# Optimization experiments

Hardware: AMD Instinct MI355X
Metric: run time of the kernel (lower is better)

The kernel has to match this reference:

```python
import jax, jax.numpy as jnp
import numpy as np

N_NODES = 100000
N_EDGES = 1600000
NFEAT, NHID, NCLASS = 512, 128, 16


def gcn_conv(x, edge_index, edge_weight, W, b):
    # Dense linear transform: [N, in] @ [in, out] -> [N, out]
    h = x @ W
    src, dst = edge_index[0], edge_index[1]
    # Edge-weighted gather + scatter-add (message passing)
    msgs = edge_weight[:, None] * h[src]            # [E, out]
    agg = jax.ops.segment_sum(msgs, dst, num_segments=x.shape[0])
    return agg + b


def setup_inputs() -> dict:
    key = jax.random.key(0)
    k = jax.random.split(key, 8)
    x = jax.random.normal(k[0], (N_NODES, NFEAT), dtype=jnp.float32)
    edge_index = jax.random.randint(k[1], (2, N_EDGES), 0, N_NODES, dtype=jnp.int64 if jax.config.jax_enable_x64 else jnp.int32)
    edge_weight = jax.random.uniform(k[2], (N_EDGES,), dtype=jnp.float32)
    # GCNConv glorot-initialized weights + zero biases
    s1 = np.sqrt(6.0 / (NFEAT + NHID)).astype(np.float32)
    s2 = np.sqrt(6.0 / (NHID + NCLASS)).astype(np.float32)
    W1 = jax.random.uniform(k[3], (NFEAT, NHID), minval=-s1, maxval=s1, dtype=jnp.float32)
    b1 = jnp.zeros((NHID,), dtype=jnp.float32)
    W2 = jax.random.uniform(k[4], (NHID, NCLASS), minval=-s2, maxval=s2, dtype=jnp.float32)
    b2 = jnp.zeros((NCLASS,), dtype=jnp.float32)
    return {"x": x, "edge_index": edge_index, "edge_weight": edge_weight,
            "W1": W1, "b1": b1, "W2": W2, "b2": b2}


def reference(x, edge_index, edge_weight, W1, b1, W2, b2):
    # GNNGuard.forward in eval mode (dropout is identity when not training)
    h = jax.nn.relu(gcn_conv(x, edge_index, edge_weight, W1, b1))
    out = gcn_conv(h, edge_index, edge_weight, W2, b2)
    return jax.nn.log_softmax(out, axis=1)
```

## Files before the change

### kernel.cpp

```cpp
#include <hip/hip_runtime.h>
#include <cstdint>
#include <cstddef>


#define NFEAT 512
#define NHID 128
#define NCLASS 16
#define MAXDEG 64
#define Q15 32768.0f
#define IQ15 3.0517578125e-05f

typedef __attribute__((ext_vector_type(8))) __bf16 bf16x8;
typedef __attribute__((ext_vector_type(4))) float f32x4;

__global__ void k_prep_w1(const float* __restrict__ W1, __bf16* __restrict__ W1f) {
    int t = blockIdx.x * 256 + threadIdx.x;
    if (t >= 16 * 8 * 64) return;
    int lane = t & 63;
    int nc = (t >> 6) & 7;
    int ks = t >> 9;
    int q = lane >> 4, col = lane & 15;
    __bf16* outp = W1f + (size_t)t * 8;
#pragma unroll
    for (int j = 0; j < 8; j++) {
        int k = ks * 32 + q * 8 + j;
        int n = nc * 16 + col;
        outp[j] = (__bf16)W1[k * NHID + n];
    }
}

__global__ void k_gemm1_scatter(const float* __restrict__ x, const __bf16* __restrict__ W1f,
                                __bf16* __restrict__ h1b, int M, int nG1, int nSc,
                                const int* __restrict__ src, const int* __restrict__ dst,
                                const float* __restrict__ ew, int* __restrict__ cnt,
                                uint32_t* __restrict__ pay, int E) {
    if ((int)blockIdx.x >= nG1) {
        int id = blockIdx.x - nG1;
        int stride = nSc << 8;
        int e0 = id * 256 + (int)threadIdx.x;
        int e1 = e0 + stride;
        bool v0 = e0 < E, v1 = e1 < E;
        int d0 = 0, s0 = 0, d1 = 0, s1 = 0;
        float w0 = 0.f, w1 = 0.f;
        if (v0) { d0 = dst[e0]; s0 = src[e0]; w0 = ew[e0]; }
        if (v1) { d1 = dst[e1]; s1 = src[e1]; w1 = ew[e1]; }
        int r0 = 0, r1 = 0;
        if (v0) r0 = atomicAdd(&cnt[d0], 1);
        if (v1) r1 = atomicAdd(&cnt[d1], 1);
        if (v0 && r0 < MAXDEG) {
            uint32_t q = (uint32_t)(w0 * Q15 + 0.5f);
            if (q > 32767u) q = 32767u;
            pay[(size_t)d0 * MAXDEG + r0] = ((uint32_t)s0 << 15) | q;
        }
        if (v1 && r1 < MAXDEG) {
            uint32_t q = (uint32_t)(w1 * Q15 + 0.5f);
            if (q > 32767u) q = 32767u;
            pay[(size_t)d1 * MAXDEG + r1] = ((uint32_t)s1 << 15) | q;
        }
        return;
    }
    int wave = threadIdx.x >> 6;
    int lane = threadIdx.x & 63;
    int q = lane >> 4;
    int col = lane & 15;
    int m0 = blockIdx.x * 64 + wave * 16 + col;
    bool valid = (m0 < M);

    f32x4 acc[8];
#pragma unroll
    for (int n = 0; n < 8; n++) acc[n] = (f32x4)(0.0f);

    const bf16x8* Bf = (const bf16x8*)W1f;
    const float* arow = x + (size_t)m0 * NFEAT + q * 8;

    for (int kk = 0; kk < NFEAT; kk += 32) {
        bf16x8 af;
        if (valid) {
            const f32x4* ap = (const f32x4*)(arow + kk);
            f32x4 a0 = __builtin_nontemporal_load(ap);
            f32x4 a1 = __builtin_nontemporal_load(ap + 1);
            af[0] = (__bf16)a0[0]; af[1] = (__bf16)a0[1];
            af[2] = (__bf16)a0[2]; af[3] = (__bf16)a0[3];
            af[4] = (__bf16)a1[0]; af[5] = (__bf16)a1[1];
            af[6] = (__bf16)a1[2]; af[7] = (__bf16)a1[3];
        } else {
#pragma unroll
            for (int j = 0; j < 8; j++) af[j] = (__bf16)0.0f;
        }
        int kb = (kk >> 5) * 8;
#pragma unroll
        for (int n = 0; n < 8; n++) {
            bf16x8 bf = Bf[(size_t)(kb + n) * 64 + lane];
            acc[n] = __builtin_amdgcn_mfma_f32_16x16x32_bf16(af, bf, acc[n], 0, 0, 0);
        }
    }

    int rbase = blockIdx.x * 64 + wave * 16 + q * 4;
#pragma unroll
    for (int r = 0; r < 4; r++) {
        int row = rbase + r;
        if (row < M) {
            __bf16* op = h1b + (size_t)row * NHID + col;
#pragma unroll
            for (int n = 0; n < 8; n++) op[n * 16] = (__bf16)acc[n][r];
        }
    }
}

__global__ void k_agg1(const uint32_t* __restrict__ h1u, const int* __restrict__ cnt,
                       const uint32_t* __restrict__ pay, const float* __restrict__ b1,
                       uint32_t* __restrict__ hu, int N) {
    int gw = (blockIdx.x * 256 + (int)threadIdx.x) >> 6;
    int lane = threadIdx.x & 63;
    if (gw >= N) return;
    const uint32_t* prow = pay + (size_t)gw * MAXDEG;
    uint32_t pv = prow[lane];
    int c = cnt[gw];
    if (c > MAXDEG) c = MAXDEG;
    int sv = (int)(pv >> 15);
    float wv = (lane < c) ? (float)(pv & 32767u) * IQ15 : 0.f;
    float ax = 0.f, ay = 0.f;
    int j = 0;
    for (; j + 8 <= c; j += 8) {
        uint32_t u[8];
        float w[8];
#pragma unroll
        for (int i = 0; i < 8; i++) {
            int s = __shfl(sv, j + i);
            w[i] = __shfl(wv, j + i);
            u[i] = h1u[(size_t)s * 64 + lane];
        }
#pragma unroll
        for (int i = 0; i < 8; i++) {
            ax = fmaf(w[i], __uint_as_float(u[i] << 16), ax);
            ay = fmaf(w[i], __uint_as_float(u[i] & 0xffff0000u), ay);
        }
    }
    for (; j + 4 <= c; j += 4) {
        uint32_t u[4];
        float w[4];
#pragma unroll
        for (int i = 0; i < 4; i++) {
            int s = __shfl(sv, j + i);
            w[i] = __shfl(wv, j + i);
            u[i] = h1u[(size_t)s * 64 + lane];
        }
#pragma unroll
        for (int i = 0; i < 4; i++) {
            ax = fmaf(w[i], __uint_as_float(u[i] << 16), ax);
            ay = fmaf(w[i], __uint_as_float(u[i] & 0xffff0000u), ay);
        }
    }
    for (; j < c; j++) {
        int s = __shfl(sv, j);
        float ww = __shfl(wv, j);
        uint32_t u = h1u[(size_t)s * 64 + lane];
        ax = fmaf(ww, __uint_as_float(u << 16), ax);
        ay = fmaf(ww, __uint_as_float(u & 0xffff0000u), ay);
    }
    float2 bb = ((const float2*)b1)[lane];
    float ox = fmaxf(ax + bb.x, 0.f);
    float oy = fmaxf(ay + bb.y, 0.f);
    union { __bf16 h[2]; uint32_t u; } cvt;
    cvt.h[0] = (__bf16)ox;
    cvt.h[1] = (__bf16)oy;
    hu[(size_t)gw * 64 + lane] = cvt.u;
}

__global__ void k_gemm2(const uint32_t* __restrict__ hu, const float* __restrict__ W2,
                        float* __restrict__ h2, int N) {
    __shared__ float W2s[NHID * NCLASS];
    __shared__ float hs[16][NHID + 4];
    int t = threadIdx.x;
#pragma unroll
    for (int j = 0; j < 8; j++) W2s[t * 8 + j] = W2[t * 8 + j];
    int nb = blockIdx.x * 16;
    {
        int idx = t * 4;
        int row = idx >> 6;
        int kp = idx & 63;
        if (nb + row < N) {
            uint4 u4 = *(const uint4*)(hu + (size_t)(nb + row) * 64 + kp);
            uint32_t us[4] = {u4.x, u4.y, u4.z, u4.w};
#pragma unroll
            for (int j = 0; j < 4; j++) {
                hs[row][(kp + j) * 2 + 0] = __uint_as_float(us[j] << 16);
                hs[row][(kp + j) * 2 + 1] = __uint_as_float(us[j] & 0xffff0000u);
            }
        } else {
#pragma unroll
            for (int j = 0; j < 4; j++) {
                hs[row][(kp + j) * 2 + 0] = 0.f;
                hs[row][(kp + j) * 2 + 1] = 0.f;
            }
        }
    }
    __syncthreads();
    int ni = t >> 4, c = t & 15;
    float acc = 0.f;
#pragma unroll 8
    for (int k = 0; k < NHID; k++) acc = fmaf(hs[ni][k], W2s[k * NCLASS + c], acc);
    if (nb + ni < N) h2[(size_t)(nb + ni) * NCLASS + c] = acc;
}

__global__ void k_agg2(const float* __restrict__ h2, const int* __restrict__ cnt,
                       const uint32_t* __restrict__ pay, const float* __restrict__ b2,
                       float* __restrict__ out, int N) {
    int gw = (blockIdx.x * 256 + (int)threadIdx.x) >> 6;
    int lane = threadIdx.x & 63;
    if (gw >= N) return;
    int c = lane & 15, eg = lane >> 4;
    const uint32_t* prow = pay + (size_t)gw * MAXDEG;
    uint32_t pv = prow[lane];
    int n = cnt[gw];
    if (n > MAXDEG) n = MAXDEG;
    int sv = (int)(pv >> 15);
    float wv = (lane < n) ? (float)(pv & 32767u) * IQ15 : 0.f;
    float acc = 0.f;
    int nr = (n + 3) >> 2;
    int i = 0;
    for (; i + 2 <= nr; i += 2) {
        int j0 = i * 4 + eg, j1 = j0 + 4;
        int s0 = __shfl(sv, j0), s1 = __shfl(sv, j1);
        float w0 = __shfl(wv, j0), w1 = __shfl(wv, j1);
        float g0 = h2[(size_t)s0 * NCLASS + c];
        float g1 = h2[(size_t)s1 * NCLASS + c];
        acc = fmaf(w0, g0, acc);
        acc = fmaf(w1, g1, acc);
    }
    if (i < nr) {
        int j0 = i * 4 + eg;
        int s0 = __shfl(sv, j0);
        float w0 = __shfl(wv, j0);
        acc = fmaf(w0, h2[(size_t)s0 * NCLASS + c], acc);
    }
    acc += __shfl_xor(acc, 16);
    acc += __shfl_xor(acc, 32);
    float o = acc + b2[c];
    float m = o;
#pragma unroll
    for (int d = 1; d < 16; d <<= 1) m = fmaxf(m, __shfl_xor(m, d));
    float e = expf(o - m);
    float ssum = e;
#pragma unroll
    for (int d = 1; d < 16; d <<= 1) ssum += __shfl_xor(ssum, d);
    if (lane < 16) out[(size_t)gw * NCLASS + c] = o - m - logf(ssum);
}

extern "C" void kernel_launch(void* const* d_in, const int* in_sizes, int n_in,
                              void* d_out, int out_size, void* d_ws, size_t ws_size,
                              hipStream_t stream) {
    const float* x  = (const float*)d_in[0];
    const int*   ei = (const int*)d_in[1];
    const float* ew = (const float*)d_in[2];
    const float* W1 = (const float*)d_in[3];
    const float* b1 = (const float*)d_in[4];
    const float* W2 = (const float*)d_in[5];
    const float* b2 = (const float*)d_in[6];
    float* out = (float*)d_out;

    int N = in_sizes[0] / NFEAT;
    int E = in_sizes[2];
    const int* srcI = ei;
    const int* dstI = ei + E;

    char* p = (char*)d_ws;
    auto alloc = [&](size_t bytes) {
        char* r = p;
        p += (bytes + 511) & ~(size_t)511;
        return r;
    };
    __bf16*   h1b  = (__bf16*)alloc((size_t)N * NHID * 2);
    uint32_t* hu   = (uint32_t*)alloc((size_t)N * (NHID / 2) * 4);
    float*    h2   = (float*)alloc((size_t)N * NCLASS * 4);
    int*      cnt  = (int*)alloc((size_t)N * 4);
    uint32_t* pay  = (uint32_t*)alloc((size_t)N * MAXDEG * 4);
    __bf16*   W1f  = (__bf16*)alloc((size_t)NFEAT * NHID * 2);

    (void)hipMemsetAsync(cnt, 0, (size_t)N * 4, stream);
    k_prep_w1<<<32, 256, 0, stream>>>(W1, W1f);

    int nG1 = (N + 63) / 64;
    int nSc = (E + 511) / 512;
    k_gemm1_scatter<<<nG1 + nSc, 256, 0, stream>>>(x, W1f, h1b, N, nG1, nSc,
                                                   srcI, dstI, ew, cnt, pay, E);

    k_agg1<<<(N + 3) / 4, 256, 0, stream>>>((const uint32_t*)h1b, cnt, pay, b1, hu, N);
    k_gemm2<<<(N + 15) / 16, 256, 0, stream>>>(hu, W2, h2, N);
    k_agg2<<<(N + 3) / 4, 256, 0, stream>>>(h2, cnt, pay, b2, out, N);
}
```

Baseline: 490.1 us.

## Process two nodes per wave in agg1 with 8-byte gathers; nontemporal payload stores

The first aggregation kernel now assigns two destination nodes to each 64-lane wave, each half-wave gathering a full 256-byte bf16 row with 8-byte loads per lane. This halves the number of waves and the per-edge shuffle and loop overhead relative to the feature work. The cost is that both halves iterate to the larger of the two degrees, with masked weights for the shorter node. Edge payload writes in the scatter phase also become nontemporal stores to reduce cache pollution.

```diff
diff --git a/kernel.cpp b/kernel.cpp
--- a/kernel.cpp
+++ b/kernel.cpp
@@ -50,12 +50,14 @@
         if (v0 && r0 < MAXDEG) {
             uint32_t q = (uint32_t)(w0 * Q15 + 0.5f);
             if (q > 32767u) q = 32767u;
-            pay[(size_t)d0 * MAXDEG + r0] = ((uint32_t)s0 << 15) | q;
+            __builtin_nontemporal_store(((uint32_t)s0 << 15) | q,
+                                        &pay[(size_t)d0 * MAXDEG + r0]);
         }
         if (v1 && r1 < MAXDEG) {
             uint32_t q = (uint32_t)(w1 * Q15 + 0.5f);
             if (q > 32767u) q = 32767u;
-            pay[(size_t)d1 * MAXDEG + r1] = ((uint32_t)s1 << 15) | q;
+            __builtin_nontemporal_store(((uint32_t)s1 << 15) | q,
+                                        &pay[(size_t)d1 * MAXDEG + r1]);
         }
         return;
     }
@@ -110,61 +112,84 @@
 __global__ void k_agg1(const uint32_t* __restrict__ h1u, const int* __restrict__ cnt,
                        const uint32_t* __restrict__ pay, const float* __restrict__ b1,
                        uint32_t* __restrict__ hu, int N) {
-    int gw = (blockIdx.x * 256 + (int)threadIdx.x) >> 6;
+    int wid = (blockIdx.x * 256 + (int)threadIdx.x) >> 6;
     int lane = threadIdx.x & 63;
-    if (gw >= N) return;
-    const uint32_t* prow = pay + (size_t)gw * MAXDEG;
-    uint32_t pv = prow[lane];
-    int c = cnt[gw];
-    if (c > MAXDEG) c = MAXDEG;
-    int sv = (int)(pv >> 15);
-    float wv = (lane < c) ? (float)(pv & 32767u) * IQ15 : 0.f;
-    float ax = 0.f, ay = 0.f;
+    int half = lane >> 5, hl = lane & 31;
+    int nA = wid * 2;
+    if (nA >= N) return;
+    int node = nA + half;
+    bool nodeValid = node < N;
+
+    uint32_t pv = nodeValid ? pay[(size_t)node * MAXDEG + hl] : 0u;
+    int c_own = 0;
+    if (nodeValid) { c_own = cnt[node]; if (c_own > MAXDEG) c_own = MAXDEG; }
+    int cA = __shfl(c_own, 0);
+    int cB = __shfl(c_own, 32);
+    int cmax = cA > cB ? cA : cB;
+    int cm32 = cmax < 32 ? cmax : 32;
+
+    const uint2* h1v = (const uint2*)h1u;
+    float a0 = 0.f, a1 = 0.f, a2 = 0.f, a3 = 0.f;
     int j = 0;
-    for (; j + 8 <= c; j += 8) {
-        uint32_t u[8];
+    for (; j + 8 <= cm32; j += 8) {
+        uint2 u[8];
         float w[8];
 #pragma unroll
         for (int i = 0; i < 8; i++) {
-            int s = __shfl(sv, j + i);
-            w[i] = __shfl(wv, j + i);
-            u[i] = h1u[(size_t)s * 64 + lane];
+            uint32_t pA = __shfl(pv, j + i);
+            uint32_t pB = __shfl(pv, 32 + j + i);
+            uint32_t p = half ? pB : pA;
+            int s = (int)(p >> 15);
+            w[i] = (j + i < c_own) ? (float)(p & 32767u) * IQ15 : 0.f;
+            u[i] = h1v[(size_t)s * 32 + hl];
         }
 #pragma unroll
         for (int i = 0; i < 8; i++) {
-            ax = fmaf(w[i], __uint_as_float(u[i] << 16), ax);
-            ay = fmaf(w[i], __uint_as_float(u[i] & 0xffff0000u), ay);
-        }
-    }
-    for (; j + 4 <= c; j += 4) {
-        uint32_t u[4];
-        float w[4];
-#pragma unroll
-        for (int i = 0; i < 4; i++) {
-            int s = __shfl(sv, j + i);
-            w[i] = __shfl(wv, j + i);
-            u[i] = h1u[(size_t)s * 64 + lane];
-        }
-#pragma unroll
-        for (int i = 0; i < 4; i++) {
-            ax = fmaf(w[i], __uint_as_float(u[i] << 16), ax);
-            ay = fmaf(w[i], __uint_as_float(u[i] & 0xffff0000u), ay);
-        }
-    }
-    for (; j < c; j++) {
-        int s = __shfl(sv, j);
-        float ww = __shfl(wv, j);
-        uint32_t u = h1u[(size_t)s * 64 + lane];
-        ax = fmaf(ww, __uint_as_float(u << 16), ax);
-        ay = fmaf(ww, __uint_as_float(u & 0xffff0000u), ay);
-    }
-    float2 bb = ((const float2*)b1)[lane];
-    float ox = fmaxf(ax + bb.x, 0.f);
-    float oy = fmaxf(ay + bb.y, 0.f);
-    union { __bf16 h[2]; uint32_t u; } cvt;
-    cvt.h[0] = (__bf16)ox;
-    cvt.h[1] = (__bf16)oy;
-    hu[(size_t)gw * 64 + lane] = cvt.u;
+            a0 = fmaf(w[i], __uint_as_float(u[i].x << 16), a0);
+            a1 = fmaf(w[i], __uint_as_float(u[i].x & 0xffff0000u), a1);
+            a2 = fmaf(w[i], __uint_as_float(u[i].y << 16), a2);
+            a3 = fmaf(w[i], __uint_as_float(u[i].y & 0xffff0000u), a3);
+        }
+    }
+    for (; j < cm32; j++) {
+        uint32_t pA = __shfl(pv, j);
+        uint32_t pB = __shfl(pv, 32 + j);
+        uint32_t p = half ? pB : pA;
+        int s = (int)(p >> 15);
+        float w = (j < c_own) ? (float)(p & 32767u) * IQ15 : 0.f;
+        uint2 u = h1v[(size_t)s * 32 + hl];
+        a0 = fmaf(w, __uint_as_float(u.x << 16), a0);
+        a1 = fmaf(w, __uint_as_float(u.x & 0xffff0000u), a1);
+        a2 = fmaf(w, __uint_as_float(u.y << 16), a2);
+        a3 = fmaf(w, __uint_as_float(u.y & 0xffff0000u), a3);
+    }
+    if (cmax > 32) {
+        uint32_t pv2 = nodeValid ? pay[(size_t)node * MAXDEG + 32 + hl] : 0u;
+        for (j = 32; j < cmax; j++) {
+            uint32_t pA = __shfl(pv2, j - 32);
+            uint32_t pB = __shfl(pv2, j);
+            uint32_t p = half ? pB : pA;
+            int s = (int)(p >> 15);
+            float w = (j < c_own) ? (float)(p & 32767u) * IQ15 : 0.f;
+            uint2 u = h1v[(size_t)s * 32 + hl];
+            a0 = fmaf(w, __uint_as_float(u.x << 16), a0);
+            a1 = fmaf(w, __uint_as_float(u.x & 0xffff0000u), a1);
+            a2 = fmaf(w, __uint_as_float(u.y << 16), a2);
+            a3 = fmaf(w, __uint_as_float(u.y & 0xffff0000u), a3);
+        }
+    }
+    if (nodeValid) {
+        float4 bb = ((const float4*)b1)[hl];
+        float o0 = fmaxf(a0 + bb.x, 0.f);
+        float o1 = fmaxf(a1 + bb.y, 0.f);
+        float o2 = fmaxf(a2 + bb.z, 0.f);
+        float o3 = fmaxf(a3 + bb.w, 0.f);
+        union { __bf16 h[2]; uint32_t u; } c0, c1;
+        c0.h[0] = (__bf16)o0; c0.h[1] = (__bf16)o1;
+        c1.h[0] = (__bf16)o2; c1.h[1] = (__bf16)o3;
+        uint2 st; st.x = c0.u; st.y = c1.u;
+        ((uint2*)hu)[(size_t)node * 32 + hl] = st;
+    }
 }
 
 __global__ void k_gemm2(const uint32_t* __restrict__ hu, const float* __restrict__ W2,
@@ -285,7 +310,8 @@
     k_gemm1_scatter<<<nG1 + nSc, 256, 0, stream>>>(x, W1f, h1b, N, nG1, nSc,
                                                    srcI, dstI, ew, cnt, pay, E);
 
-    k_agg1<<<(N + 3) / 4, 256, 0, stream>>>((const uint32_t*)h1b, cnt, pay, b1, hu, N);
+    k_agg1<<<((N + 1) / 2 * 64 + 255) / 256, 256, 0, stream>>>(
+        (const uint32_t*)h1b, cnt, pay, b1, hu, N);
     k_gemm2<<<(N + 15) / 16, 256, 0, stream>>>(hu, W2, h2, N);
     k_agg2<<<(N + 3) / 4, 256, 0, stream>>>(h2, cnt, pay, b2, out, N);
 }
```

Result: no change. 495.6 us (+1.1%).
